# Kernel optimization log

Measured on AMD Instinct MI355X. Metric: run time of the kernel, lower is better.

Reference implementation:

```python
import jax, jax.numpy as jnp
import numpy as np

T, B, IN, H, L = 512, 256, 64, 128, 5  # seq, batch, in_dim, hidden, layers


def _lstm_layer(x_seq, W_ih, W_hh, b_ih, b_hh):
    # x_seq: [T, B, D]; W_ih: [4H, D]; W_hh: [4H, H]; biases: [4H]
    # Precompute input contribution for all timesteps (big GEMM, compute-dense)
    pre = jnp.einsum('tbd,gd->tbg', x_seq, W_ih) + b_ih + b_hh  # [T, B, 4H]
    h0 = jnp.zeros((x_seq.shape[1], W_hh.shape[1]), x_seq.dtype)
    c0 = h0

    def step(carry, p):
        h, c = carry
        gates = p + h @ W_hh.T  # [B, 4H], PyTorch gate order i,f,g,o
        i, f, g, o = jnp.split(gates, 4, axis=-1)
        i = jax.nn.sigmoid(i)
        f = jax.nn.sigmoid(f)
        g = jnp.tanh(g)
        o = jax.nn.sigmoid(o)
        c = f * c + i * g
        h = o * jnp.tanh(c)
        return (h, c), h

    _, hs = jax.lax.scan(step, (h0, c0), pre)
    return hs  # [T, B, H]


def setup_inputs() -> dict:
    key = jax.random.key(0)
    ks = jax.random.split(key, 6)
    s = 1.0 / np.sqrt(H)  # PyTorch LSTM init scale
    return {
        'x': jax.random.normal(ks[0], (T, B, IN), jnp.float32),
        'W_ih0': jax.random.uniform(ks[1], (4 * H, IN), jnp.float32, -s, s),
        'W_ih_rest': jax.random.uniform(ks[2], (L - 1, 4 * H, H), jnp.float32, -s, s),
        'W_hh': jax.random.uniform(ks[3], (L, 4 * H, H), jnp.float32, -s, s),
        'b_ih': jax.random.uniform(ks[4], (L, 4 * H), jnp.float32, -s, s),
        'b_hh': jax.random.uniform(ks[5], (L, 4 * H), jnp.float32, -s, s),
    }


def reference(x, W_ih0, W_ih_rest, W_hh, b_ih, b_hh):
    # 5-layer stacked LSTM, eval mode (inter-layer dropout inactive).
    h = _lstm_layer(x, W_ih0, W_hh[0], b_ih[0], b_hh[0])
    for l in range(1, L):  # fixed small layer loop
        h = _lstm_layer(h, W_ih_rest[l - 1], W_hh[l], b_ih[l], b_hh[l])
    return h  # [T, B, H]
```

## Files before the change

kernel.cpp:

```cpp
#include <hip/hip_runtime.h>


typedef unsigned short ushort_t;
typedef unsigned int uint_t;
typedef unsigned long long ull_t;
typedef __attribute__((ext_vector_type(8))) short short8;
typedef __attribute__((ext_vector_type(4))) float floatx4;
typedef __attribute__((ext_vector_type(2))) float floatx2;

#define T_STEPS 512
#define BATCH   256
#define HID     128
#define NL      5
#define NBG     16
#define RING_R  64
#define PRIME   24
#define FLAG_STRIDE 16
#define SLOT_U  (BATCH * HID / 2)
#define RING_U  ((size_t)RING_R * SLOT_U)
#define WS_NEED (8192 + 4 * RING_U * 4)
#define LDS_BYTES 98304

__device__ __forceinline__ ushort_t f2bf(float f) {
  unsigned int u = __float_as_uint(f);
  u += 0x7FFF + ((u >> 16) & 1);
  return (ushort_t)(u >> 16);
}
__device__ __forceinline__ float sigm(float x) {
  float e = __builtin_amdgcn_exp2f(-1.442695041f * x);
  return __builtin_amdgcn_rcpf(1.0f + e);
}
__device__ __forceinline__ float tanh_(float x) {
  float e = __builtin_amdgcn_exp2f(-2.885390082f * x);
  float s = __builtin_amdgcn_rcpf(1.0f + e);
  return __builtin_fmaf(2.0f, s, -1.0f);
}
__device__ __forceinline__ int flag_ld(const int* p) {
  return __hip_atomic_load(p, __ATOMIC_RELAXED, __HIP_MEMORY_SCOPE_AGENT);
}
__device__ __forceinline__ ull_t ring_ld8(const uint_t* base, int tid) {
  return __hip_atomic_load((const ull_t*)base + tid, __ATOMIC_RELAXED,
                           __HIP_MEMORY_SCOPE_AGENT);
}
__device__ __forceinline__ void ring_st8(uint_t* base, int tid, ull_t v) {
  __hip_atomic_store((ull_t*)base + tid, v, __ATOMIC_RELAXED,
                     __HIP_MEMORY_SCOPE_AGENT);
}

__global__ void init_flags(int* flags) {
  int i = blockIdx.x * 256 + threadIdx.x;
  if (i < NL * NBG * FLAG_STRIDE)
    __hip_atomic_store(&flags[i], 0, __ATOMIC_RELAXED,
                       __HIP_MEMORY_SCOPE_AGENT);
}

template <int KIN, bool SRC_F32, bool RING_OUT>
__device__ __forceinline__ void lstm_stage(
    unsigned char* lds,
    const float* xf32,
    const uint_t* ring_in,
    const float* __restrict__ Wih, const float* __restrict__ Whh,
    const float* __restrict__ bih, const float* __restrict__ bhh,
    uint_t* ring_out,
    float* out_f32,
    int* up_flag, int* down_flag, int* my_flag, int bg)
{
  constexpr int KX = KIN / 32, KT = KX + 4;
  constexpr int XS = KIN + 8;
  constexpr int HS = 128 + 8;

  typedef ushort_t (*XT)[16][XS];
  typedef ushort_t (*HT)[16][HS];
  XT Xr = (XT)lds;
  HT Hr = (HT)(lds + (size_t)8 * 16 * XS * 2);
  int* upm = (int*)(lds + (size_t)8 * 16 * XS * 2 + (size_t)2 * 16 * HS * 2);
  int* dnm = upm + 4;

  const int tid  = threadIdx.x;
  const int wave = tid >> 6;
  const int lane = tid & 63;
  const int col  = lane & 15;
  const int quad = lane >> 4;
  const int j    = wave * 16 + col;
  const int frow = tid >> 5;
  const int fc   = tid & 31;

  for (int i = tid; i < 2 * 16 * HS; i += 512) (&Hr[0][0][0])[i] = 0;
  if (tid == 0) {
#pragma unroll
    for (int i = 0; i < 4; ++i) { upm[i] = 0; dnm[i] = 0; }
  }

  short8 wf[4][KT];
#pragma unroll
  for (int nt = 0; nt < 4; ++nt) {
    int n = nt * 128 + j;
#pragma unroll
    for (int kt = 0; kt < KX; ++kt) {
      const float* p = Wih + n * KIN + kt * 32 + quad * 8;
      short8 w;
#pragma unroll
      for (int e = 0; e < 8; ++e) w[e] = (short)f2bf(p[e]);
      wf[nt][kt] = w;
    }
#pragma unroll
    for (int kt = 0; kt < 4; ++kt) {
      const float* p = Whh + n * 128 + kt * 32 + quad * 8;
      short8 w;
#pragma unroll
      for (int e = 0; e < 8; ++e) w[e] = (short)f2bf(p[e]);
      wf[nt][KX + kt] = w;
    }
  }
  const float bi  = bih[j]       + bhh[j];
  const float bf_ = bih[128 + j] + bhh[128 + j];
  const float bgi = bih[256 + j] + bhh[256 + j];
  const float bo  = bih[384 + j] + bhh[384 + j];

  floatx4 c = {0.f, 0.f, 0.f, 0.f};
  int pu = 0, pd = 0;
  ull_t  pf4[4];
  floatx2 px4[4];

  __syncthreads();

  if constexpr (!SRC_F32) {
    int v = 0;
    while ((v = flag_ld(up_flag)) < PRIME) __builtin_amdgcn_s_sleep(1);
    asm volatile("" ::: "memory");
    if (tid == 0) {
#pragma unroll
      for (int i = 0; i < 4; ++i) upm[i] = v;
      pu = v;
    }
    ull_t pr[8];
#pragma unroll
    for (int s = 0; s < 8; ++s)
      pr[s] = ring_ld8(ring_in + (size_t)s * SLOT_U + bg * 1024, tid);
#pragma unroll
    for (int s = 0; s < 8; ++s)
      *(ull_t*)(&Xr[s][frow][fc * 4]) = pr[s];
  } else {
    floatx2 pr[8];
#pragma unroll
    for (int s = 0; s < 8; ++s)
      pr[s] = *(const floatx2*)(xf32 +
                                ((size_t)s * BATCH + bg * 16 + frow) * 64 +
                                fc * 2);
#pragma unroll
    for (int s = 0; s < 8; ++s)
      *(uint_t*)(&Xr[s][frow][fc * 2]) =
          (uint_t)f2bf(pr[s][0]) | ((uint_t)f2bf(pr[s][1]) << 16);
  }
  asm volatile("s_waitcnt lgkmcnt(0)\n\ts_barrier" ::: "memory");

  for (int t = 0; t < T_STEPS; ++t) {
    if ((t & 3) == 0) {
      if (t >= 4) {
        asm volatile("s_waitcnt vmcnt(0)\n\ts_barrier" ::: "memory");
        if (tid == 0)
          __hip_atomic_store(my_flag, t - 1, __ATOMIC_RELAXED,
                             __HIP_MEMORY_SCOPE_AGENT);
#pragma unroll
        for (int g = 0; g < 4; ++g) {
          const int s = t + 4 + g;
          if (s < T_STEPS) {
            if constexpr (SRC_F32)
              *(uint_t*)(&Xr[s & 7][frow][fc * 2]) =
                  (uint_t)f2bf(px4[g][0]) | ((uint_t)f2bf(px4[g][1]) << 16);
            else
              *(ull_t*)(&Xr[s & 7][frow][fc * 4]) = pf4[g];
          }
        }
      }
      if (t + 8 < T_STEPS) {
        if constexpr (!SRC_F32) {
          int need = t + 12;
          if (need > T_STEPS) need = T_STEPS;
          if (upm[t & 3] < need) {
            while (flag_ld(up_flag) < need) __builtin_amdgcn_s_sleep(1);
          }
        }
        asm volatile("" ::: "memory");
#pragma unroll
        for (int g = 0; g < 4; ++g) {
          const int s = t + 8 + g;
          if (s < T_STEPS) {
            if constexpr (SRC_F32)
              px4[g] = *(const floatx2*)(
                  xf32 + ((size_t)s * BATCH + bg * 16 + frow) * 64 + fc * 2);
            else
              pf4[g] = ring_ld8(
                  ring_in + (size_t)(s & (RING_R - 1)) * SLOT_U + bg * 1024,
                  tid);
          }
        }
      }
    }
    const int dn = dnm[t & 3];

    if constexpr (RING_OUT) {
      if (t >= 1) {
        const int s = t - 1;
        if (s - dn > RING_R - 16) {
          while (s - flag_ld(down_flag) > RING_R - 16)
            __builtin_amdgcn_s_sleep(1);
          asm volatile("" ::: "memory");
        }
        ull_t h8 = *(const ull_t*)(&Hr[t & 1][frow][fc * 4]);
        ring_st8(ring_out + (size_t)(s & (RING_R - 1)) * SLOT_U + bg * 1024,
                 tid, h8);
      }
    }

    short8 af[KT];
#pragma unroll
    for (int kt = 0; kt < KX; ++kt)
      af[kt] = *(const short8*)(&Xr[t & 7][col][kt * 32 + quad * 8]);
#pragma unroll
    for (int kt = 0; kt < 4; ++kt)
      af[KX + kt] = *(const short8*)(&Hr[t & 1][col][kt * 32 + quad * 8]);
    floatx4 a0 = {0, 0, 0, 0}, a1 = {0, 0, 0, 0}, a2 = {0, 0, 0, 0},
            a3 = {0, 0, 0, 0};
#pragma unroll
    for (int kt = 0; kt < KT; ++kt) {
      short8 a = af[kt];
      a0 = __builtin_amdgcn_mfma_f32_16x16x32_bf16(a, wf[0][kt], a0, 0, 0, 0);
      a1 = __builtin_amdgcn_mfma_f32_16x16x32_bf16(a, wf[1][kt], a1, 0, 0, 0);
      a2 = __builtin_amdgcn_mfma_f32_16x16x32_bf16(a, wf[2][kt], a2, 0, 0, 0);
      a3 = __builtin_amdgcn_mfma_f32_16x16x32_bf16(a, wf[3][kt], a3, 0, 0, 0);
    }

    if (tid == 0) {
      if constexpr (!SRC_F32) {
        upm[(t + 2) & 3] = pu;
        pu = flag_ld(up_flag);
      }
      if constexpr (RING_OUT) {
        dnm[(t + 2) & 3] = pd;
        pd = flag_ld(down_flag);
      }
    }

    ushort_t (*wr)[HS] = Hr[(t & 1) ^ 1];
#pragma unroll
    for (int r = 0; r < 4; ++r) {
      float iv = sigm(a0[r] + bi);
      float fv = sigm(a1[r] + bf_);
      float gv = tanh_(a2[r] + bgi);
      float ov = sigm(a3[r] + bo);
      float cn = __builtin_fmaf(fv, c[r], iv * gv);
      c[r] = cn;
      float hv = ov * tanh_(cn);
      wr[quad * 4 + r][j] = f2bf(hv);
      if constexpr (!RING_OUT) {
        out_f32[((size_t)t * BATCH + bg * 16 + quad * 4 + r) * HID + j] = hv;
      }
    }

    asm volatile("s_waitcnt lgkmcnt(0)\n\ts_barrier" ::: "memory");
  }

  if constexpr (RING_OUT) {
    const int s = T_STEPS - 1;
    while (s - flag_ld(down_flag) > RING_R - 16) __builtin_amdgcn_s_sleep(1);
    asm volatile("" ::: "memory");
    ull_t h8 = *(const ull_t*)(&Hr[T_STEPS & 1][frow][fc * 4]);
    ring_st8(ring_out + (size_t)(s & (RING_R - 1)) * SLOT_U + bg * 1024, tid,
             h8);
  }
  asm volatile("s_waitcnt vmcnt(0)\n\ts_barrier" ::: "memory");
  if (tid == 0)
    __hip_atomic_store(my_flag, T_STEPS, __ATOMIC_RELAXED,
                       __HIP_MEMORY_SCOPE_AGENT);
}

__global__ __launch_bounds__(512) void lstm_pipe(
    const float* x, const float* Wih0, const float* WihR,
    const float* Whh, const float* bih, const float* bhh,
    float* out, uint_t* ring, int* flags)
{
  __shared__ __align__(16) unsigned char lds_raw[LDS_BYTES];
  const int l  = blockIdx.x >> 4;
  const int bg = blockIdx.x & 15;
  int* mine = flags + (l * NBG + bg) * FLAG_STRIDE;
  int* up   = (l > 0) ? flags + ((l - 1) * NBG + bg) * FLAG_STRIDE : nullptr;
  int* down = (l < 4) ? flags + ((l + 1) * NBG + bg) * FLAG_STRIDE : nullptr;

  if (l == 0) {
    lstm_stage<64, true, true>(lds_raw, x, nullptr, Wih0, Whh, bih, bhh,
                               ring, nullptr, up, down, mine, bg);
  } else if (l < 4) {
    lstm_stage<128, false, true>(lds_raw, nullptr,
                                 ring + (size_t)(l - 1) * RING_U,
                                 WihR + (size_t)(l - 1) * 512 * 128,
                                 Whh + (size_t)l * 512 * 128,
                                 bih + l * 512, bhh + l * 512,
                                 ring + (size_t)l * RING_U, nullptr,
                                 up, down, mine, bg);
  } else {
    lstm_stage<128, false, false>(lds_raw, nullptr,
                                  ring + (size_t)3 * RING_U,
                                  WihR + (size_t)3 * 512 * 128,
                                  Whh + (size_t)4 * 512 * 128,
                                  bih + 4 * 512, bhh + 4 * 512,
                                  nullptr, out, up, nullptr, mine, bg);
  }
}

template <int KIN>
__global__ __launch_bounds__(512) void lstm_layer(
    const float* xin, float* hout,
    const float* __restrict__ Wih, const float* __restrict__ Whh,
    const float* __restrict__ bih, const float* __restrict__ bhh)
{
  constexpr int KX = KIN / 32, KT = KX + 4;
  constexpr int AW = KIN + 128, AS = AW + 8;
  constexpr int NSTG = 16 * KIN / 4;

  const int bg = blockIdx.x, tid = threadIdx.x;
  const int wave = tid >> 6, lane = tid & 63;
  const int col = lane & 15, quad = lane >> 4;
  const int j = wave * 16 + col;

  __shared__ __align__(16) ushort_t Ah[2][16][AS];
  for (int i = tid; i < 2 * 16 * AS; i += 512) (&Ah[0][0][0])[i] = 0;

  short8 wf[4][KT];
#pragma unroll
  for (int nt = 0; nt < 4; ++nt) {
    int n = nt * 128 + j;
#pragma unroll
    for (int kt = 0; kt < KX; ++kt) {
      const float* p = Wih + n * KIN + kt * 32 + quad * 8;
      short8 w;
#pragma unroll
      for (int e = 0; e < 8; ++e) w[e] = (short)f2bf(p[e]);
      wf[nt][kt] = w;
    }
#pragma unroll
    for (int kt = 0; kt < 4; ++kt) {
      const float* p = Whh + n * 128 + kt * 32 + quad * 8;
      short8 w;
#pragma unroll
      for (int e = 0; e < 8; ++e) w[e] = (short)f2bf(p[e]);
      wf[nt][KX + kt] = w;
    }
  }
  const float bi  = bih[j]       + bhh[j];
  const float bf_ = bih[128 + j] + bhh[128 + j];
  const float bgi = bih[256 + j] + bhh[256 + j];
  const float bo  = bih[384 + j] + bhh[384 + j];

  floatx4 c = {0.f, 0.f, 0.f, 0.f};
  const int srow = tid / (KIN / 4), scol = (tid % (KIN / 4)) * 4;
  floatx4 xv = {0.f, 0.f, 0.f, 0.f};
  auto stage_load = [&](int t) {
    if (tid < NSTG && t < T_STEPS)
      xv = *(const floatx4*)(xin + (size_t)(t * BATCH + bg * 16 + srow) * KIN + scol);
  };
  auto stage_store = [&](int t, ushort_t (*buf)[AS]) {
    if (tid < NSTG && t < T_STEPS) {
#pragma unroll
      for (int e = 0; e < 4; ++e) buf[srow][scol + e] = f2bf(xv[e]);
    }
  };
  __syncthreads();
  stage_load(0); stage_store(0, Ah[0]); stage_load(1);
  __syncthreads();

  for (int t = 0; t < T_STEPS; ++t) {
    ushort_t (*rd)[AS] = Ah[t & 1];
    ushort_t (*wr)[AS] = Ah[(t & 1) ^ 1];
    short8 af[KT];
#pragma unroll
    for (int kt = 0; kt < KT; ++kt)
      af[kt] = *(const short8*)(&rd[col][kt * 32 + quad * 8]);
    floatx4 a0 = {0, 0, 0, 0}, a1 = {0, 0, 0, 0}, a2 = {0, 0, 0, 0},
            a3 = {0, 0, 0, 0};
#pragma unroll
    for (int kt = 0; kt < KT; ++kt) {
      short8 a = af[kt];
      a0 = __builtin_amdgcn_mfma_f32_16x16x32_bf16(a, wf[0][kt], a0, 0, 0, 0);
      a1 = __builtin_amdgcn_mfma_f32_16x16x32_bf16(a, wf[1][kt], a1, 0, 0, 0);
      a2 = __builtin_amdgcn_mfma_f32_16x16x32_bf16(a, wf[2][kt], a2, 0, 0, 0);
      a3 = __builtin_amdgcn_mfma_f32_16x16x32_bf16(a, wf[3][kt], a3, 0, 0, 0);
    }
    stage_store(t + 1, wr);
    stage_load(t + 2);
    size_t obase = (size_t)(t * BATCH + bg * 16) * HID + j;
#pragma unroll
    for (int r = 0; r < 4; ++r) {
      int row = quad * 4 + r;
      float iv = sigm(a0[r] + bi);
      float fv = sigm(a1[r] + bf_);
      float gv = tanh_(a2[r] + bgi);
      float ov = sigm(a3[r] + bo);
      float cn = __builtin_fmaf(fv, c[r], iv * gv);
      c[r] = cn;
      float hv = ov * tanh_(cn);
      wr[row][KIN + j] = f2bf(hv);
      hout[obase + (size_t)row * HID] = hv;
    }
    __syncthreads();
  }
}

extern "C" void kernel_launch(void* const* d_in, const int* in_sizes, int n_in,
                              void* d_out, int out_size, void* d_ws,
                              size_t ws_size, hipStream_t stream) {
  const float* x    = (const float*)d_in[0];
  const float* Wih0 = (const float*)d_in[1];
  const float* WihR = (const float*)d_in[2];
  const float* Whh  = (const float*)d_in[3];
  const float* bih  = (const float*)d_in[4];
  const float* bhh  = (const float*)d_in[5];
  float* out = (float*)d_out;

  if (ws_size >= WS_NEED) {
    int* flags = (int*)d_ws;
    uint_t* ring = (uint_t*)((char*)d_ws + 8192);
    init_flags<<<(NL * NBG * FLAG_STRIDE + 255) / 256, 256, 0, stream>>>(flags);
    lstm_pipe<<<NL * NBG, 512, 0, stream>>>(x, Wih0, WihR, Whh, bih, bhh,
                                            out, ring, flags);
  } else {
    lstm_layer<64><<<16, 512, 0, stream>>>(x, out, Wih0, Whh, bih, bhh);
    for (int l = 1; l < 5; ++l)
      lstm_layer<128><<<16, 512, 0, stream>>>(
          out, out, WihR + (size_t)(l - 1) * 512 * 128,
          Whh + (size_t)l * 512 * 128, bih + l * 512, bhh + l * 512);
  }
}
```

Before: 896.5 us.

## Precompute next step's input-projection MFMAs off the recurrent critical path

Splits the per-step gate GEMM into the input-projection part (X times W_ih) and the recurrent part (h times W_hh). The input part for step t+1 is issued after step t's recurrent MFMAs, so it can overlap the activation math, and the bias is folded into the accumulator initialisation. A ping-pong pair of accumulator arrays with a 2x unrolled loop keeps register indexing static. This shortens the dependency chain from h to the next h, at the cost of extra live accumulator registers and a correctness dependence on Xr[t+1] already being resident when it is read.

```diff
diff --git a/kernel.cpp b/kernel.cpp
--- a/kernel.cpp
+++ b/kernel.cpp
@@ -121,6 +121,7 @@
   int pu = 0, pd = 0;
   ull_t  pf4[4];
   floatx2 px4[4];
+  floatx4 pA[4], pB[4];
 
   __syncthreads();
 
@@ -154,7 +155,20 @@
   }
   asm volatile("s_waitcnt lgkmcnt(0)\n\ts_barrier" ::: "memory");
 
-  for (int t = 0; t < T_STEPS; ++t) {
+  pA[0] = (floatx4){bi, bi, bi, bi};
+  pA[1] = (floatx4){bf_, bf_, bf_, bf_};
+  pA[2] = (floatx4){bgi, bgi, bgi, bgi};
+  pA[3] = (floatx4){bo, bo, bo, bo};
+#pragma unroll
+  for (int kt = 0; kt < KX; ++kt) {
+    short8 ax = *(const short8*)(&Xr[0][col][kt * 32 + quad * 8]);
+    pA[0] = __builtin_amdgcn_mfma_f32_16x16x32_bf16(ax, wf[0][kt], pA[0], 0, 0, 0);
+    pA[1] = __builtin_amdgcn_mfma_f32_16x16x32_bf16(ax, wf[1][kt], pA[1], 0, 0, 0);
+    pA[2] = __builtin_amdgcn_mfma_f32_16x16x32_bf16(ax, wf[2][kt], pA[2], 0, 0, 0);
+    pA[3] = __builtin_amdgcn_mfma_f32_16x16x32_bf16(ax, wf[3][kt], pA[3], 0, 0, 0);
+  }
+
+  auto body = [&](int t, floatx4 (&pc)[4], floatx4 (&pn)[4]) {
     if ((t & 3) == 0) {
       if (t >= 4) {
         asm volatile("s_waitcnt vmcnt(0)\n\ts_barrier" ::: "memory");
@@ -213,22 +227,28 @@
       }
     }
 
-    short8 af[KT];
-#pragma unroll
-    for (int kt = 0; kt < KX; ++kt)
-      af[kt] = *(const short8*)(&Xr[t & 7][col][kt * 32 + quad * 8]);
-#pragma unroll
-    for (int kt = 0; kt < 4; ++kt)
-      af[KX + kt] = *(const short8*)(&Hr[t & 1][col][kt * 32 + quad * 8]);
-    floatx4 a0 = {0, 0, 0, 0}, a1 = {0, 0, 0, 0}, a2 = {0, 0, 0, 0},
-            a3 = {0, 0, 0, 0};
-#pragma unroll
-    for (int kt = 0; kt < KT; ++kt) {
-      short8 a = af[kt];
-      a0 = __builtin_amdgcn_mfma_f32_16x16x32_bf16(a, wf[0][kt], a0, 0, 0, 0);
-      a1 = __builtin_amdgcn_mfma_f32_16x16x32_bf16(a, wf[1][kt], a1, 0, 0, 0);
-      a2 = __builtin_amdgcn_mfma_f32_16x16x32_bf16(a, wf[2][kt], a2, 0, 0, 0);
-      a3 = __builtin_amdgcn_mfma_f32_16x16x32_bf16(a, wf[3][kt], a3, 0, 0, 0);
+#pragma unroll
+    for (int kt = 0; kt < 4; ++kt) {
+      short8 a = *(const short8*)(&Hr[t & 1][col][kt * 32 + quad * 8]);
+      pc[0] = __builtin_amdgcn_mfma_f32_16x16x32_bf16(a, wf[0][KX + kt], pc[0], 0, 0, 0);
+      pc[1] = __builtin_amdgcn_mfma_f32_16x16x32_bf16(a, wf[1][KX + kt], pc[1], 0, 0, 0);
+      pc[2] = __builtin_amdgcn_mfma_f32_16x16x32_bf16(a, wf[2][KX + kt], pc[2], 0, 0, 0);
+      pc[3] = __builtin_amdgcn_mfma_f32_16x16x32_bf16(a, wf[3][KX + kt], pc[3], 0, 0, 0);
+    }
+
+    if (t + 1 < T_STEPS) {
+      pn[0] = (floatx4){bi, bi, bi, bi};
+      pn[1] = (floatx4){bf_, bf_, bf_, bf_};
+      pn[2] = (floatx4){bgi, bgi, bgi, bgi};
+      pn[3] = (floatx4){bo, bo, bo, bo};
+#pragma unroll
+      for (int kt = 0; kt < KX; ++kt) {
+        short8 ax = *(const short8*)(&Xr[(t + 1) & 7][col][kt * 32 + quad * 8]);
+        pn[0] = __builtin_amdgcn_mfma_f32_16x16x32_bf16(ax, wf[0][kt], pn[0], 0, 0, 0);
+        pn[1] = __builtin_amdgcn_mfma_f32_16x16x32_bf16(ax, wf[1][kt], pn[1], 0, 0, 0);
+        pn[2] = __builtin_amdgcn_mfma_f32_16x16x32_bf16(ax, wf[2][kt], pn[2], 0, 0, 0);
+        pn[3] = __builtin_amdgcn_mfma_f32_16x16x32_bf16(ax, wf[3][kt], pn[3], 0, 0, 0);
+      }
     }
 
     if (tid == 0) {
@@ -245,10 +265,10 @@
     ushort_t (*wr)[HS] = Hr[(t & 1) ^ 1];
 #pragma unroll
     for (int r = 0; r < 4; ++r) {
-      float iv = sigm(a0[r] + bi);
-      float fv = sigm(a1[r] + bf_);
-      float gv = tanh_(a2[r] + bgi);
-      float ov = sigm(a3[r] + bo);
+      float iv = sigm(pc[0][r]);
+      float fv = sigm(pc[1][r]);
+      float gv = tanh_(pc[2][r]);
+      float ov = sigm(pc[3][r]);
       float cn = __builtin_fmaf(fv, c[r], iv * gv);
       c[r] = cn;
       float hv = ov * tanh_(cn);
@@ -259,6 +279,11 @@
     }
 
     asm volatile("s_waitcnt lgkmcnt(0)\n\ts_barrier" ::: "memory");
+  };
+
+  for (int t = 0; t < T_STEPS; t += 2) {
+    body(t, pA, pB);
+    body(t + 1, pB, pA);
   }
 
   if constexpr (RING_OUT) {
```

After: 863.1 us. 3.7% less time.
